# Optimization experiments

Measured on AMD Instinct MI355X. Metric: run time of the kernel, lower is better.

## Reference

```python
import jax, jax.numpy as jnp
import numpy as np

MAX_DISP = 4
STRIDE = 2

def setup_inputs() -> dict:
    key = jax.random.key(0)
    k1, k2 = jax.random.split(key)
    B, C, H, W = 8, 256, 96, 192
    in1 = jax.random.normal(k1, (B, C, H, W), dtype=jnp.float32)
    in2 = jax.random.normal(k2, (B, C, H, W), dtype=jnp.float32)
    return {"in1": in1, "in2": in2}

def reference(in1, in2):
    # Correlation (cost volume) layer: for each displacement (dy, dx) on a
    # stride-2 grid in [-max_disp, max_disp], compute channel-mean of
    # in1 * shifted(in2). Output: [B, D^2, H, W] with D = max_disp/stride*2 + 1.
    B, C, H, W = in1.shape
    md, st = MAX_DISP, STRIDE
    in2p = jnp.pad(in2, ((0, 0), (0, 0), (md, md), (md, md)))  # zero pad H, W
    offsets = range(0, 2 * md + 1, st)  # {0,2,4,6,8} -> 5 per axis
    # dy outer, dx inner matches torch.meshgrid('ij') flatten order.
    corr = [jnp.mean(in1 * in2p[:, :, dy:dy + H, dx:dx + W], axis=1)
            for dy in offsets for dx in offsets]
    return jnp.stack(corr, axis=1)  # [B, 25, H, W]
```

## Files before the change

### kernel.cpp

```cpp
#include <hip/hip_runtime.h>

#define BB 8
#define CH 256
#define HH 96
#define WW 192
#define HW (HH*WW)
#define ND 25
#define TH 32
#define TW 64
#define S2H 40
#define S2W 72
#define S2SLOTS (S2H*S2W/4)
#define NTHR 512
#define OUTSZ (BB*ND*HH*WW)

__global__ __launch_bounds__(NTHR, 2)
void corr_partial(const float* __restrict__ in1, const float* __restrict__ in2,
                  float* __restrict__ part, int cCount) {
  __shared__ float s2[2][S2H*S2W];

  const int tile = blockIdx.x;
  const int b    = tile / 9;
  const int rem  = tile - b*9;
  const int h0   = (rem / 3) * TH;
  const int w0   = (rem % 3) * TW;
  const int t    = threadIdx.x;
  const int r    = t >> 4;
  const int c0   = (t & 15) << 2;

  const int cBegin = blockIdx.y * cCount;

  const size_t bplane = (size_t)b * CH * HW;
  const float* in1b = in1 + bplane;
  const float* in2b = in2 + bplane;

  const int s0row = t / 18, s0c4 = t - (t/18)*18;
  const int g0r = h0 + s0row - 4, g0c = w0 + (s0c4 << 2) - 4;
  const bool v0 = ((unsigned)g0r < HH) & ((unsigned)g0c <= (unsigned)(WW-4));
  const float* src0 = in2b + (size_t)cBegin*HW + (v0 ? (g0r*WW + g0c) : 0);
  const int lofs0 = s0row*S2W + (s0c4 << 2);

  const int t1 = t + NTHR;
  const bool has1 = t1 < S2SLOTS;
  const int s1row = t1 / 18, s1c4 = t1 - (t1/18)*18;
  const int g1r = h0 + s1row - 4, g1c = w0 + (s1c4 << 2) - 4;
  const bool v1 = has1 & ((unsigned)g1r < HH) & ((unsigned)g1c <= (unsigned)(WW-4));
  const float* src1 = in2b + (size_t)cBegin*HW + (v1 ? (g1r*WW + g1c) : 0);
  const int lofs1 = has1 ? (s1row*S2W + (s1c4 << 2)) : lofs0;

  const float* p1 = in1b + (size_t)cBegin*HW + (h0 + r)*WW + (w0 + c0);

  float4 acc[ND];
  #pragma unroll
  for (int d = 0; d < ND; ++d) acc[d] = make_float4(0.f, 0.f, 0.f, 0.f);
  const float4 z4 = make_float4(0.f, 0.f, 0.f, 0.f);

  {
    float4 x0 = v0 ? *(const float4*)src0 : z4;
    *(float4*)&s2[0][lofs0] = x0;
    if (has1) {
      float4 x1 = v1 ? *(const float4*)src1 : z4;
      *(float4*)&s2[0][lofs1] = x1;
    }
  }
  float4 a = *(const float4*)p1;
  __syncthreads();

  for (int cc = 0; cc < cCount; ++cc) {
    const int cur = cc & 1;
    float4 sv0 = z4, sv1 = z4, an = z4;
    const bool more = (cc + 1) < cCount;
    if (more) {
      const size_t adv = (size_t)(cc + 1) * HW;
      if (v0) sv0 = *(const float4*)(src0 + adv);
      if (v1) sv1 = *(const float4*)(src1 + adv);
      an = *(const float4*)(p1 + adv);
    }
    const float* sbase = &s2[cur][0];
    #pragma unroll
    for (int dyi = 0; dyi < 5; ++dyi) {
      const float* rowp = sbase + (r + 2*dyi)*S2W + c0;
      float wv[12];
      *(float4*)&wv[0] = *(const float4*)(rowp);
      *(float4*)&wv[4] = *(const float4*)(rowp + 4);
      *(float4*)&wv[8] = *(const float4*)(rowp + 8);
      #pragma unroll
      for (int dxi = 0; dxi < 5; ++dxi) {
        float4& A = acc[dyi*5 + dxi];
        A.x = fmaf(a.x, wv[0 + 2*dxi], A.x);
        A.y = fmaf(a.y, wv[1 + 2*dxi], A.y);
        A.z = fmaf(a.z, wv[2 + 2*dxi], A.z);
        A.w = fmaf(a.w, wv[3 + 2*dxi], A.w);
      }
    }
    if (more) {
      float* dbase = &s2[cur ^ 1][0];
      *(float4*)(dbase + lofs0) = sv0;
      if (has1) *(float4*)(dbase + lofs1) = sv1;
      a = an;
    }
    __syncthreads();
  }

  const float scale = 1.0f / CH;
  float* pout = part + (size_t)blockIdx.y * OUTSZ
              + ((size_t)b*ND*HH + (h0 + r))*WW + (w0 + c0);
  #pragma unroll
  for (int d = 0; d < ND; ++d) {
    float4 v;
    v.x = acc[d].x * scale; v.y = acc[d].y * scale;
    v.z = acc[d].z * scale; v.w = acc[d].w * scale;
    *(float4*)(pout + (size_t)d*HW) = v;
  }
}

__global__ void corr_reduce(const float* __restrict__ part,
                            float* __restrict__ out, int G) {
  const int n4 = OUTSZ / 4;
  int i = blockIdx.x * 256 + threadIdx.x;
  if (i >= n4) return;
  const float4* p = (const float4*)part;
  float4 s = p[i];
  for (int g = 1; g < G; ++g) {
    float4 v = p[(size_t)g * n4 + i];
    s.x += v.x; s.y += v.y; s.z += v.z; s.w += v.w;
  }
  ((float4*)out)[i] = s;
}

extern "C" void kernel_launch(void* const* d_in, const int* in_sizes, int n_in,
                              void* d_out, int out_size, void* d_ws, size_t ws_size,
                              hipStream_t stream) {
  const float* in1 = (const float*)d_in[0];
  const float* in2 = (const float*)d_in[1];
  float* out = (float*)d_out;

  int G = 4;
  while (G > 1 && ws_size < (size_t)G * OUTSZ * sizeof(float)) G >>= 1;
  float* part = (G == 1) ? out : (float*)d_ws;

  dim3 grid(BB * 9, G);
  corr_partial<<<grid, NTHR, 0, stream>>>(in1, in2, part, CH / G);
  if (G > 1) {
    corr_reduce<<<(OUTSZ/4 + 255)/256, 256, 0, stream>>>((const float*)d_ws, out, G);
  }
}
```

Before: 180.7 us.

## Split each block into two channel halves with in-block shared-memory reduction

Halves the spatial tile height to 16 rows and lets the two 256-thread halves of each block work on disjoint channel ranges, each with its own double-buffered shared tile. At the end, the second half writes its accumulators to shared memory in chunks and the first half adds them, scales, and stores. This doubles the block count (144 per channel group) to spread work over more CUs, but it increases the halo overhead per output and adds extra synchronisation in the epilogue.

```diff
diff --git a/kernel.cpp b/kernel.cpp
--- a/kernel.cpp
+++ b/kernel.cpp
@@ -6,47 +6,49 @@
 #define WW 192
 #define HW (HH*WW)
 #define ND 25
-#define TH 32
+#define TH 16
 #define TW 64
-#define S2H 40
+#define S2H 24
 #define S2W 72
-#define S2SLOTS (S2H*S2W/4)
+#define S2Q (S2H*S2W/4)
 #define NTHR 512
 #define OUTSZ (BB*ND*HH*WW)
 
 __global__ __launch_bounds__(NTHR, 2)
 void corr_partial(const float* __restrict__ in1, const float* __restrict__ in2,
-                  float* __restrict__ part, int cCount) {
-  __shared__ float s2[2][S2H*S2W];
+                  float* __restrict__ part, int cPerHalf, int G) {
+  __shared__ __align__(16) float smem[2][2][S2H*S2W];
 
   const int tile = blockIdx.x;
-  const int b    = tile / 9;
-  const int rem  = tile - b*9;
+  const int b    = tile / 18;
+  const int rem  = tile - b*18;
   const int h0   = (rem / 3) * TH;
   const int w0   = (rem % 3) * TW;
   const int t    = threadIdx.x;
-  const int r    = t >> 4;
-  const int c0   = (t & 15) << 2;
+  const int half = t >> 8;
+  const int ti   = t & 255;
+  const int r    = ti >> 4;
+  const int c0   = (ti & 15) << 2;
 
-  const int cBegin = blockIdx.y * cCount;
+  const int cBegin = blockIdx.y * (cPerHalf * 2) + half * cPerHalf;
 
   const size_t bplane = (size_t)b * CH * HW;
   const float* in1b = in1 + bplane;
   const float* in2b = in2 + bplane;
 
-  const int s0row = t / 18, s0c4 = t - (t/18)*18;
-  const int g0r = h0 + s0row - 4, g0c = w0 + (s0c4 << 2) - 4;
+  const int s0row = ti / 18, s0q = ti - (ti/18)*18;
+  const int g0r = h0 + s0row - 4, g0c = w0 + (s0q << 2) - 4;
   const bool v0 = ((unsigned)g0r < HH) & ((unsigned)g0c <= (unsigned)(WW-4));
   const float* src0 = in2b + (size_t)cBegin*HW + (v0 ? (g0r*WW + g0c) : 0);
-  const int lofs0 = s0row*S2W + (s0c4 << 2);
+  const int lofs0 = s0row*S2W + (s0q << 2);
 
-  const int t1 = t + NTHR;
-  const bool has1 = t1 < S2SLOTS;
-  const int s1row = t1 / 18, s1c4 = t1 - (t1/18)*18;
-  const int g1r = h0 + s1row - 4, g1c = w0 + (s1c4 << 2) - 4;
+  const int t1 = ti + 256;
+  const bool has1 = t1 < S2Q;
+  const int s1row = t1 / 18, s1q = t1 - (t1/18)*18;
+  const int g1r = h0 + s1row - 4, g1c = w0 + (s1q << 2) - 4;
   const bool v1 = has1 & ((unsigned)g1r < HH) & ((unsigned)g1c <= (unsigned)(WW-4));
   const float* src1 = in2b + (size_t)cBegin*HW + (v1 ? (g1r*WW + g1c) : 0);
-  const int lofs1 = has1 ? (s1row*S2W + (s1c4 << 2)) : lofs0;
+  const int lofs1 = has1 ? (s1row*S2W + (s1q << 2)) : lofs0;
 
   const float* p1 = in1b + (size_t)cBegin*HW + (h0 + r)*WW + (w0 + c0);
 
@@ -57,26 +59,26 @@
 
   {
     float4 x0 = v0 ? *(const float4*)src0 : z4;
-    *(float4*)&s2[0][lofs0] = x0;
+    *(float4*)&smem[half][0][lofs0] = x0;
     if (has1) {
       float4 x1 = v1 ? *(const float4*)src1 : z4;
-      *(float4*)&s2[0][lofs1] = x1;
+      *(float4*)&smem[half][0][lofs1] = x1;
     }
   }
   float4 a = *(const float4*)p1;
   __syncthreads();
 
-  for (int cc = 0; cc < cCount; ++cc) {
+  for (int cc = 0; cc < cPerHalf; ++cc) {
     const int cur = cc & 1;
     float4 sv0 = z4, sv1 = z4, an = z4;
-    const bool more = (cc + 1) < cCount;
+    const bool more = (cc + 1) < cPerHalf;
     if (more) {
       const size_t adv = (size_t)(cc + 1) * HW;
       if (v0) sv0 = *(const float4*)(src0 + adv);
       if (v1) sv1 = *(const float4*)(src1 + adv);
       an = *(const float4*)(p1 + adv);
     }
-    const float* sbase = &s2[cur][0];
+    const float* sbase = &smem[half][cur][0];
     #pragma unroll
     for (int dyi = 0; dyi < 5; ++dyi) {
       const float* rowp = sbase + (r + 2*dyi)*S2W + c0;
@@ -94,7 +96,7 @@
       }
     }
     if (more) {
-      float* dbase = &s2[cur ^ 1][0];
+      float* dbase = &smem[half][cur ^ 1][0];
       *(float4*)(dbase + lofs0) = sv0;
       if (has1) *(float4*)(dbase + lofs1) = sv1;
       a = an;
@@ -103,14 +105,29 @@
   }
 
   const float scale = 1.0f / CH;
+  float4* red = (float4*)&smem[0][0][0];
   float* pout = part + (size_t)blockIdx.y * OUTSZ
               + ((size_t)b*ND*HH + (h0 + r))*WW + (w0 + c0);
-  #pragma unroll
-  for (int d = 0; d < ND; ++d) {
-    float4 v;
-    v.x = acc[d].x * scale; v.y = acc[d].y * scale;
-    v.z = acc[d].z * scale; v.w = acc[d].w * scale;
-    *(float4*)(pout + (size_t)d*HW) = v;
+  for (int ch5 = 0; ch5 < 5; ++ch5) {
+    if (half == 1) {
+      #pragma unroll
+      for (int dd = 0; dd < 5; ++dd) red[dd*256 + ti] = acc[ch5*5 + dd];
+    }
+    __syncthreads();
+    if (half == 0) {
+      #pragma unroll
+      for (int dd = 0; dd < 5; ++dd) {
+        const int d = ch5*5 + dd;
+        float4 v = red[dd*256 + ti];
+        float4 o;
+        o.x = (acc[d].x + v.x) * scale;
+        o.y = (acc[d].y + v.y) * scale;
+        o.z = (acc[d].z + v.z) * scale;
+        o.w = (acc[d].w + v.w) * scale;
+        *(float4*)(pout + (size_t)d*HW) = o;
+      }
+    }
+    __syncthreads();
   }
 }
 
@@ -139,8 +156,8 @@
   while (G > 1 && ws_size < (size_t)G * OUTSZ * sizeof(float)) G >>= 1;
   float* part = (G == 1) ? out : (float*)d_ws;
 
-  dim3 grid(BB * 9, G);
-  corr_partial<<<grid, NTHR, 0, stream>>>(in1, in2, part, CH / G);
+  dim3 grid(BB * 18, G);
+  corr_partial<<<grid, NTHR, 0, stream>>>(in1, in2, part, CH / (G * 2), G);
   if (G > 1) {
     corr_reduce<<<(OUTSZ/4 + 255)/256, 256, 0, stream>>>((const float*)d_ws, out, G);
   }
```

Measured after the change: 153.0 us. -15.3%, faster.
